# Kernel optimization log

Measured on AMD Instinct MI355X. Metric: run time of the kernel, lower is better.

## Reference

```python
import jax, jax.numpy as jnp
import numpy as np

N = 20000       # n_nodes
NHID = 256      # nhid_gcn
NOUT = 128      # gcn output / gru input
H = 128         # nout_gru
NHID_E = 256    # nhid_edges
T = 16          # snapshots (end_day - start_day + 1)
E = 320000      # edges per snapshot
EP = 100000     # edges to predict
BN_EPS = 1e-5


def setup_inputs() -> dict:
    key = jax.random.key(0)
    ks = jax.random.split(key, 20)
    s = 0.02
    return {
        "adj_rows": jax.random.randint(ks[0], (T, E), 0, N, dtype=jnp.int32),
        "adj_cols": jax.random.randint(ks[1], (T, E), 0, N, dtype=jnp.int32),
        "adj_vals": jax.random.uniform(ks[2], (T, E), dtype=jnp.float32),
        "edges": jax.random.randint(ks[3], (2, EP), 0, N, dtype=jnp.int32),
        # GCN params (layer0: nfeat=N -> NHID, layer1: NHID -> NOUT)
        "W0": jax.random.normal(ks[4], (N, NHID), jnp.float32) * s,
        "b0": jnp.zeros((NHID,), jnp.float32),
        "W1": jax.random.normal(ks[5], (NHID, NOUT), jnp.float32) * s,
        "b1": jnp.zeros((NOUT,), jnp.float32),
        # GRU params (torch layout: [3H, in], [3H, H])
        "W_ih": jax.random.normal(ks[6], (3 * H, NOUT), jnp.float32) * s,
        "W_hh": jax.random.normal(ks[7], (3 * H, H), jnp.float32) * s,
        "b_ih": jnp.zeros((3 * H,), jnp.float32),
        "b_hh": jnp.zeros((3 * H,), jnp.float32),
        # BatchNorm1d affine params
        "gamma": jnp.ones((H,), jnp.float32),
        "beta": jnp.zeros((H,), jnp.float32),
        # edge predictor MLP
        "We1": jax.random.normal(ks[8], (2 * H, NHID_E), jnp.float32) * s,
        "be1": jnp.full((NHID_E,), 0.01, jnp.float32),
        "We2": jax.random.normal(ks[9], (NHID_E, 2), jnp.float32) * s,
        "be2": jnp.full((2,), 0.01, jnp.float32),
    }


def reference(adj_rows, adj_cols, adj_vals, edges,
              W0, b0, W1, b1, W_ih, W_hh, b_ih, b_hh,
              gamma, beta, We1, be1, We2, be2):
    def spmm(rows, cols, vals, x):
        # (sparse adj) @ x via gather + segment_sum  -> [N, d]
        return jax.ops.segment_sum(vals[:, None] * x[cols], rows, num_segments=N)

    def gcn_step(rows, cols, vals):
        # layer 0: input is identity, so support = W0
        x = spmm(rows, cols, vals, W0) + b0
        x = jax.nn.relu(x)              # dropout p=0.0 -> no-op
        # layer 1 (output layer, no relu)
        x = spmm(rows, cols, vals, x @ W1) + b1
        return x

    out = jax.vmap(gcn_step)(adj_rows, adj_cols, adj_vals)  # [T, N, NOUT]

    # single-layer GRU over time, batch = nodes
    def gru_cell(h, x):
        gi = x @ W_ih.T + b_ih
        gh = h @ W_hh.T + b_hh
        i_r, i_z, i_n = jnp.split(gi, 3, axis=-1)
        h_r, h_z, h_n = jnp.split(gh, 3, axis=-1)
        r = jax.nn.sigmoid(i_r + h_r)
        z = jax.nn.sigmoid(i_z + h_z)
        n = jnp.tanh(i_n + r * h_n)
        return (1.0 - z) * n + z * h, None

    h0 = jnp.zeros((N, H), out.dtype)
    final_emb, _ = jax.lax.scan(gru_cell, h0, out)  # [N, H]

    # BatchNorm1d in training mode: batch (node) statistics, biased variance
    mean = final_emb.mean(axis=0)
    var = final_emb.var(axis=0)
    final_emb = (final_emb - mean) * jax.lax.rsqrt(var + BN_EPS) * gamma + beta

    nodes_first = final_emb[edges[0]]
    nodes_second = final_emb[edges[1]]
    hcat = jnp.concatenate([nodes_first, nodes_second], axis=1)  # [EP, 2H]
    hmid = jax.nn.relu(hcat @ We1 + be1)
    logits = hmid @ We2 + be2
    return jax.nn.log_softmax(logits, axis=1)
```

## Files before the change

### kernel.cpp

```cpp
#include <hip/hip_runtime.h>
#include <math.h>

#define N_NODES 20000
#define NHID    256
#define NOUT    128
#define HDIM    128
#define NHID_E  256
#define T_SNAP  16
#define E_EDGES 320000
#define EP_EDGES 100000
#define BN_EPS  1e-5f

#define BROWS 128
#define NBUCK 157
#define BCAP  4096
#define P1CHUNK 2048

typedef unsigned short u16;
typedef __attribute__((ext_vector_type(8))) short bf16x8;
typedef __attribute__((ext_vector_type(8))) unsigned short u16x8;
typedef __attribute__((ext_vector_type(4))) float f32x4;

__device__ __forceinline__ u16 f2b(float f) {
    unsigned u = __float_as_uint(f);
    u += 0x7FFFu + ((u >> 16) & 1u);
    return (u16)(u >> 16);
}
__device__ __forceinline__ float b2f(u16 s) { return __uint_as_float(((unsigned)s) << 16); }

__device__ __forceinline__ float fexp2(float x) {
#if __has_builtin(__builtin_amdgcn_exp2f)
    return __builtin_amdgcn_exp2f(x);
#else
    return exp2f(x);
#endif
}
__device__ __forceinline__ float frcp(float x) {
#if __has_builtin(__builtin_amdgcn_rcpf)
    return __builtin_amdgcn_rcpf(x);
#else
    return 1.f / x;
#endif
}
__device__ __forceinline__ float fsig(float x) {
    return frcp(1.f + fexp2(x * -1.4426950408889634f));
}
__device__ __forceinline__ float ftanh(float x) {
    float t = fexp2(x * 2.8853900817779268f);
    return 1.f - 2.f * frcp(t + 1.f);
}

#if __has_builtin(__builtin_amdgcn_fdot2_f32_bf16)
#define HAVE_DOT2 1
typedef __attribute__((ext_vector_type(2))) __bf16 bf2v;
__device__ __forceinline__ float dot2b(unsigned x, unsigned v, float acc) {
    return __builtin_amdgcn_fdot2_f32_bf16(
        __builtin_bit_cast(bf2v, x), __builtin_bit_cast(bf2v, v), acc, false);
}
__device__ __forceinline__ unsigned pack_lo(unsigned a, unsigned b) {
#if __has_builtin(__builtin_amdgcn_perm)
    return __builtin_amdgcn_perm(a, b, 0x01000504u);
#else
    return (a & 0xFFFFu) | (b << 16);
#endif
}
__device__ __forceinline__ unsigned pack_hi(unsigned a, unsigned b) {
#if __has_builtin(__builtin_amdgcn_perm)
    return __builtin_amdgcn_perm(a, b, 0x03020706u);
#else
    return (a >> 16) | (b & 0xFFFF0000u);
#endif
}
#else
#define HAVE_DOT2 0
#endif

__global__ __launch_bounds__(256) void k_p1(const int* __restrict__ rows,
        const int* __restrict__ cols, const float* __restrict__ vals,
        int* __restrict__ bcnt, uint2* __restrict__ staging,
        uint4* __restrict__ ovf, int* __restrict__ ovf_cnt) {
    int t = blockIdx.y;
    int base = blockIdx.x * P1CHUNK;
    int tid = threadIdx.x;
    __shared__ int hist[256], sc[256], excl[256], cursor[256], gbase[256];
    __shared__ uint2 ebuf[P1CHUNK];
    __shared__ u16 ebuck[P1CHUNK];
    hist[tid] = 0;
    __syncthreads();
    const int*   rt = rows + (size_t)t * E_EDGES;
    const int*   ct = cols + (size_t)t * E_EDGES;
    const float* vt = vals + (size_t)t * E_EDGES;
    #pragma unroll
    for (int k = 0; k < P1CHUNK / 256; ++k) {
        int i = base + k * 256 + tid;
        if (i < E_EDGES) atomicAdd(&hist[rt[i] >> 7], 1);
    }
    __syncthreads();
    sc[tid] = hist[tid];
    __syncthreads();
    for (int off = 1; off < 256; off <<= 1) {
        int add = (tid >= off) ? sc[tid - off] : 0;
        __syncthreads();
        sc[tid] += add;
        __syncthreads();
    }
    excl[tid]   = sc[tid] - hist[tid];
    cursor[tid] = sc[tid] - hist[tid];
    __syncthreads();
    #pragma unroll
    for (int k = 0; k < P1CHUNK / 256; ++k) {
        int i = base + k * 256 + tid;
        if (i < E_EDGES) {
            int r = rt[i];
            int b = r >> 7;
            int s = atomicAdd(&cursor[b], 1);
            uint2 e;
            e.x = (unsigned)ct[i] | ((unsigned)(r & 127) << 15);
            e.y = __float_as_uint(vt[i]);
            ebuf[s]  = e;
            ebuck[s] = (u16)b;
        }
    }
    __syncthreads();
    if (hist[tid] > 0) gbase[tid] = atomicAdd(&bcnt[t * NBUCK + tid], hist[tid]);
    __syncthreads();
    int nvalid = min(P1CHUNK, E_EDGES - base);
    for (int s = tid; s < nvalid; s += 256) {
        int b = ebuck[s];
        int g = gbase[b] + (s - excl[b]);
        if (g < BCAP) {
            staging[((size_t)t * NBUCK + b) * BCAP + g] = ebuf[s];
        } else {
            int o = atomicAdd(ovf_cnt, 1);
            uint4 e4; e4.x = (unsigned)(t * NBUCK + b); e4.y = ebuf[s].x; e4.z = ebuf[s].y; e4.w = 0;
            ovf[o] = e4;
        }
    }
}

__global__ void k_bscan(const int* __restrict__ bcnt, int* __restrict__ bbase,
                        int* __restrict__ row_ptr) {
    __shared__ int sh[256];
    __shared__ int carry;
    int tid = threadIdx.x;
    if (tid == 0) carry = 0;
    __syncthreads();
    for (int b0 = 0; b0 < T_SNAP * NBUCK; b0 += 256) {
        int i = b0 + tid;
        int v = (i < T_SNAP * NBUCK) ? bcnt[i] : 0;
        sh[tid] = v;
        __syncthreads();
        for (int off = 1; off < 256; off <<= 1) {
            int add = (tid >= off) ? sh[tid - off] : 0;
            __syncthreads();
            sh[tid] += add;
            __syncthreads();
        }
        if (i < T_SNAP * NBUCK) bbase[i] = carry + sh[tid] - v;
        __syncthreads();
        if (tid == 255) carry += sh[255];
        __syncthreads();
    }
    if (tid < T_SNAP) row_ptr[tid * (N_NODES + 1) + N_NODES] = E_EDGES;
}

__global__ __launch_bounds__(256) void k_p2(const int* __restrict__ bcnt,
        const int* __restrict__ bbase, const uint2* __restrict__ staging,
        const uint4* __restrict__ ovf, const int* __restrict__ ovf_cnt,
        uint2* __restrict__ colval, int* __restrict__ row_ptr) {
    int b = blockIdx.x, t = blockIdx.y, tid = threadIdx.x;
    int idx = t * NBUCK + b;
    int cnt = bcnt[idx];
    int gb  = bbase[idx];
    __shared__ int hist[BROWS], cursor[BROWS], sc[BROWS];
    if (tid < BROWS) hist[tid] = 0;
    __syncthreads();
    int staged = min(cnt, BCAP);
    const uint2* st = staging + (size_t)idx * BCAP;
    for (int s = tid; s < staged; s += 256)
        atomicAdd(&hist[st[s].x >> 15], 1);
    int nov = (cnt > staged) ? *ovf_cnt : 0;
    for (int o = tid; o < nov; o += 256) {
        uint4 e = ovf[o];
        if ((int)e.x == idx) atomicAdd(&hist[(e.y >> 15) & 127], 1);
    }
    __syncthreads();
    if (tid < BROWS) sc[tid] = hist[tid];
    __syncthreads();
    for (int off = 1; off < BROWS; off <<= 1) {
        int add = (tid < BROWS && tid >= off) ? sc[tid - off] : 0;
        __syncthreads();
        if (tid < BROWS) sc[tid] += add;
        __syncthreads();
    }
    if (tid < BROWS) {
        int ex = sc[tid] - hist[tid];
        cursor[tid] = ex;
        int row = b * BROWS + tid;
        if (row < N_NODES)
            row_ptr[t * (N_NODES + 1) + row] = gb - t * E_EDGES + ex;
    }
    __syncthreads();
    for (int s = tid; s < staged; s += 256) {
        uint2 e = st[s];
        int rl = e.x >> 15;
        int pos = atomicAdd(&cursor[rl], 1);
        uint2 o2; o2.x = e.x & 0x7FFF; o2.y = e.y;
        colval[(size_t)gb + pos] = o2;
    }
    for (int o = tid; o < nov; o += 256) {
        uint4 e = ovf[o];
        if ((int)e.x == idx) {
            int rl = (e.y >> 15) & 127;
            int pos = atomicAdd(&cursor[rl], 1);
            uint2 o2; o2.x = e.y & 0x7FFF; o2.y = e.z;
            colval[(size_t)gb + pos] = o2;
        }
    }
}

__global__ void k_cvt(const float* __restrict__ in, u16* __restrict__ out, int n4) {
    int i = blockIdx.x * 256 + threadIdx.x;
    if (i < n4) {
        float4 v = ((const float4*)in)[i];
        ushort4 o;
        o.x = f2b(v.x); o.y = f2b(v.y); o.z = f2b(v.z); o.w = f2b(v.w);
        ((ushort4*)out)[i] = o;
    }
}

__global__ void k_tcvt(const float* __restrict__ in, u16* __restrict__ out, int Kr, int Nc) {
    int i = blockIdx.x * 256 + threadIdx.x;
    if (i < Kr * Nc) {
        int k = i / Nc, n = i - k * Nc;
        out[(size_t)n * Kr + k] = f2b(in[i]);
    }
}

__global__ void k_build_bg(const float* __restrict__ Wih, const float* __restrict__ Whh,
                           u16* __restrict__ Bg) {
    int i = blockIdx.x * 256 + threadIdx.x;
    if (i >= 512 * 256) return;
    int rr = i >> 8, k = i & 255;
    int c = rr >> 4, u = rr & 15, g = c & 3, jj = ((c >> 2) << 4) + u;
    float v;
    if (g == 0)      v = (k < 128) ? Wih[(size_t)jj * 128 + k]         : Whh[(size_t)jj * 128 + k - 128];
    else if (g == 1) v = (k < 128) ? Wih[(size_t)(128 + jj) * 128 + k] : Whh[(size_t)(128 + jj) * 128 + k - 128];
    else if (g == 2) v = (k < 128) ? Wih[(size_t)(256 + jj) * 128 + k] : 0.f;
    else             v = (k < 128) ? 0.f : Whh[(size_t)(256 + jj) * 128 + k - 128];
    Bg[i] = f2b(v);
}

__global__ void k_build_bgb(const float* __restrict__ bih, const float* __restrict__ bhh,
                            float* __restrict__ bgb) {
    int rr = blockIdx.x * 256 + threadIdx.x;
    if (rr >= 512) return;
    int c = rr >> 4, u = rr & 15, g = c & 3, jj = ((c >> 2) << 4) + u;
    float v;
    if (g == 0)      v = bih[jj] + bhh[jj];
    else if (g == 1) v = bih[128 + jj] + bhh[128 + jj];
    else if (g == 2) v = bih[256 + jj];
    else             v = bhh[256 + jj];
    bgb[rr] = v;
}

template<bool RELU>
__global__ __launch_bounds__(256) void k_spmm0(
        const int* __restrict__ rp_all, const uint2* __restrict__ cv_all,
        int t0, const u16* __restrict__ X,
        const float* __restrict__ bias, u16* __restrict__ Out) {
    int lane = threadIdx.x & 63;
    int row = blockIdx.x * 4 + (threadIdx.x >> 6);
    int tl = blockIdx.y, t = t0 + tl;
    const int*   rp = rp_all + (size_t)t * (N_NODES + 1);
    const uint2* cv = cv_all + (size_t)t * E_EDGES;
    int hw = lane >> 5, l = lane & 31;
    int s = rp[row], e = rp[row + 1];
    int k = s + hw;
    uint2 a0 = make_uint2(0u, 0u), a1 = make_uint2(0u, 0u);
    if (k < e)     a0 = cv[k];
    if (k + 2 < e) a1 = cv[k + 2];
#if HAVE_DOT2
    float acc[8] = {};
    for (; k < e; k += 4) {
        uint2 c0 = a0, c1 = a1;
        bool ok1 = (k + 2) < e;
        int e1 = e - 1;
        a0 = cv[min(k + 4, e1)];
        a1 = cv[min(k + 6, e1)];
        unsigned col1 = ok1 ? c1.x : c0.x;
        float va1f = ok1 ? __uint_as_float(c1.y) : 0.f;
        unsigned vv = (unsigned)f2b(__uint_as_float(c0.y)) | ((unsigned)f2b(va1f) << 16);
        uint4 x0 = *(const uint4*)(X + (size_t)c0.x * NHID + l * 8);
        uint4 x1 = *(const uint4*)(X + (size_t)col1 * NHID + l * 8);
        acc[0] = dot2b(pack_lo(x0.x, x1.x), vv, acc[0]);
        acc[1] = dot2b(pack_hi(x0.x, x1.x), vv, acc[1]);
        acc[2] = dot2b(pack_lo(x0.y, x1.y), vv, acc[2]);
        acc[3] = dot2b(pack_hi(x0.y, x1.y), vv, acc[3]);
        acc[4] = dot2b(pack_lo(x0.z, x1.z), vv, acc[4]);
        acc[5] = dot2b(pack_hi(x0.z, x1.z), vv, acc[5]);
        acc[6] = dot2b(pack_lo(x0.w, x1.w), vv, acc[6]);
        acc[7] = dot2b(pack_hi(x0.w, x1.w), vv, acc[7]);
    }
    #pragma unroll
    for (int i = 0; i < 8; ++i) {
        float v = acc[i];
        v += __shfl_xor(v, 32);
        v += bias[l * 8 + i];
        acc[i] = RELU ? fmaxf(v, 0.f) : v;
    }
    float* accw = acc;
#else
    float acc0[8] = {}, acc1[8] = {};
    for (; k < e; k += 4) {
        uint2 c0 = a0, c1 = a1;
        bool ok1 = (k + 2) < e;
        int e1 = e - 1;
        a0 = cv[min(k + 4, e1)];
        a1 = cv[min(k + 6, e1)];
        float va0 = __uint_as_float(c0.y);
        float va1 = ok1 ? __uint_as_float(c1.y) : 0.f;
        unsigned col1 = ok1 ? c1.x : c0.x;
        u16x8 x0 = *(const u16x8*)(X + (size_t)c0.x * NHID + l * 8);
        u16x8 x1 = *(const u16x8*)(X + (size_t)col1 * NHID + l * 8);
        #pragma unroll
        for (int i = 0; i < 8; ++i) {
            acc0[i] = fmaf(va0, b2f(x0[i]), acc0[i]);
            acc1[i] = fmaf(va1, b2f(x1[i]), acc1[i]);
        }
    }
    #pragma unroll
    for (int i = 0; i < 8; ++i) {
        float v = acc0[i] + acc1[i];
        v += __shfl_xor(v, 32);
        v += bias[l * 8 + i];
        acc0[i] = RELU ? fmaxf(v, 0.f) : v;
    }
    float* accw = acc0;
#endif
    if (hw == 0) {
        u16x8 o;
        #pragma unroll
        for (int i = 0; i < 8; ++i) o[i] = f2b(accw[i]);
        *(u16x8*)(Out + ((size_t)tl * N_NODES + row) * NHID + l * 8) = o;
    }
}

template<bool RELU>
__global__ __launch_bounds__(256) void k_spmm1(
        const int* __restrict__ rp_all, const uint2* __restrict__ cv_all,
        int t0, const u16* __restrict__ X, size_t xtstride,
        const float* __restrict__ bias, u16* __restrict__ Out) {
    int lane = threadIdx.x & 63;
    int row = blockIdx.x * 4 + (threadIdx.x >> 6);
    int tl = blockIdx.y, t = t0 + tl;
    const int*   rp = rp_all + (size_t)t * (N_NODES + 1);
    const uint2* cv = cv_all + (size_t)t * E_EDGES;
    const u16*   Xt = X + xtstride * tl;
    int qw = lane >> 4, l = lane & 15;
    int s = rp[row], e = rp[row + 1];
    int k = s + qw;
    uint2 a0 = make_uint2(0u, 0u), a1 = make_uint2(0u, 0u);
    if (k < e)     a0 = cv[k];
    if (k + 4 < e) a1 = cv[k + 4];
#if HAVE_DOT2
    float acc[8] = {};
    for (; k < e; k += 8) {
        uint2 c0 = a0, c1 = a1;
        bool ok1 = (k + 4) < e;
        int e1 = e - 1;
        a0 = cv[min(k + 8, e1)];
        a1 = cv[min(k + 12, e1)];
        unsigned col1 = ok1 ? c1.x : c0.x;
        float va1f = ok1 ? __uint_as_float(c1.y) : 0.f;
        unsigned vv = (unsigned)f2b(__uint_as_float(c0.y)) | ((unsigned)f2b(va1f) << 16);
        uint4 x0 = *(const uint4*)(Xt + (size_t)c0.x * NOUT + l * 8);
        uint4 x1 = *(const uint4*)(Xt + (size_t)col1 * NOUT + l * 8);
        acc[0] = dot2b(pack_lo(x0.x, x1.x), vv, acc[0]);
        acc[1] = dot2b(pack_hi(x0.x, x1.x), vv, acc[1]);
        acc[2] = dot2b(pack_lo(x0.y, x1.y), vv, acc[2]);
        acc[3] = dot2b(pack_hi(x0.y, x1.y), vv, acc[3]);
        acc[4] = dot2b(pack_lo(x0.z, x1.z), vv, acc[4]);
        acc[5] = dot2b(pack_hi(x0.z, x1.z), vv, acc[5]);
        acc[6] = dot2b(pack_lo(x0.w, x1.w), vv, acc[6]);
        acc[7] = dot2b(pack_hi(x0.w, x1.w), vv, acc[7]);
    }
    #pragma unroll
    for (int i = 0; i < 8; ++i) {
        float v = acc[i];
        v += __shfl_xor(v, 32);
        v += __shfl_xor(v, 16);
        v += bias[l * 8 + i];
        acc[i] = RELU ? fmaxf(v, 0.f) : v;
    }
    float* accw = acc;
#else
    float acc0[8] = {}, acc1[8] = {};
    for (; k < e; k += 8) {
        uint2 c0 = a0, c1 = a1;
        bool ok1 = (k + 4) < e;
        int e1 = e - 1;
        a0 = cv[min(k + 8, e1)];
        a1 = cv[min(k + 12, e1)];
        float va0 = __uint_as_float(c0.y);
        float va1 = ok1 ? __uint_as_float(c1.y) : 0.f;
        unsigned col1 = ok1 ? c1.x : c0.x;
        u16x8 x0 = *(const u16x8*)(Xt + (size_t)c0.x * NOUT + l * 8);
        u16x8 x1 = *(const u16x8*)(Xt + (size_t)col1 * NOUT + l * 8);
        #pragma unroll
        for (int i = 0; i < 8; ++i) {
            acc0[i] = fmaf(va0, b2f(x0[i]), acc0[i]);
            acc1[i] = fmaf(va1, b2f(x1[i]), acc1[i]);
        }
    }
    #pragma unroll
    for (int i = 0; i < 8; ++i) {
        float v = acc0[i] + acc1[i];
        v += __shfl_xor(v, 32);
        v += __shfl_xor(v, 16);
        v += bias[l * 8 + i];
        acc0[i] = RELU ? fmaxf(v, 0.f) : v;
    }
    float* accw = acc0;
#endif
    if (qw == 0) {
        u16x8 o;
        #pragma unroll
        for (int i = 0; i < 8; ++i) o[i] = f2b(accw[i]);
        *(u16x8*)(Out + ((size_t)tl * N_NODES + row) * NOUT + l * 8) = o;
    }
}

template<int KC, bool BIAS>
__global__ __launch_bounds__(256) void k_mgemm(
        const u16* __restrict__ A, const u16* __restrict__ B, int ldb,
        const float* __restrict__ bias, u16* __restrict__ C, int ldc, int M) {
    constexpr int K = KC * 32;
    __shared__ bf16x8 frag[8 * KC * 64];
    int tid = threadIdx.x, lane = tid & 63, wave = tid >> 6;
    int m0 = blockIdx.y * 64, n0 = blockIdx.x * 128;

    for (int f = wave; f < 8 * KC; f += 4) {
        int nl = f / KC, kc = f % KC;
        frag[f * 64 + lane] = *(const bf16x8*)(B + (size_t)(n0 + nl * 16 + (lane & 15)) * ldb
                                               + kc * 32 + ((lane >> 4) << 3));
    }
    __syncthreads();

    int arow = m0 + wave * 16 + (lane & 15);
    bool rowok = arow < M;
    const u16* ap = A + (size_t)arow * K + ((lane >> 4) << 3);
    bf16x8 zf = {0, 0, 0, 0, 0, 0, 0, 0};
    bf16x8 af[KC];
    #pragma unroll
    for (int kc = 0; kc < KC; ++kc)
        af[kc] = rowok ? *(const bf16x8*)(ap + kc * 32) : zf;

    f32x4 acc[8] = {};
    #pragma unroll
    for (int kc = 0; kc < KC; ++kc)
        #pragma unroll
        for (int nl = 0; nl < 8; ++nl)
            acc[nl] = __builtin_amdgcn_mfma_f32_16x16x32_bf16(
                af[kc], frag[(nl * KC + kc) * 64 + lane], acc[nl], 0, 0, 0);

    int r0 = m0 + wave * 16 + ((lane >> 4) << 2);
    #pragma unroll
    for (int nl = 0; nl < 8; ++nl) {
        int col = n0 + nl * 16 + (lane & 15);
        float bv = BIAS ? bias[col] : 0.f;
        #pragma unroll
        for (int r = 0; r < 4; ++r) {
            int row = r0 + r;
            if (row < M) C[(size_t)row * ldc + col] = f2b(acc[nl][r] + bv);
        }
    }
}

__global__ __launch_bounds__(512, 2) void k_gru_fused2(
        const u16* __restrict__ X2_all, const u16* __restrict__ Bg,
        const float* __restrict__ bgb, float* __restrict__ H) {
    __shared__ u16 hbuf[2][32][132];
    int tid = threadIdx.x, lane = tid & 63, wave = tid >> 6;
    int q = wave >> 1, hb = wave & 1;
    int u = lane & 15, kgrp = lane >> 4;
    int m0 = blockIdx.x * 32;
    int jj = (2 * q + hb) * 16 + u;

    bf16x8 bfrag[4][8];
    #pragma unroll
    for (int g = 0; g < 4; ++g)
        #pragma unroll
        for (int kc = 0; kc < 8; ++kc)
            bfrag[g][kc] = *(const bf16x8*)(Bg
                + (size_t)(q * 128 + (4 * hb + g) * 16 + u) * 256
                + kc * 32 + kgrp * 8);

    float bR = bgb[q * 128 + (4 * hb + 0) * 16 + u];
    float bZ = bgb[q * 128 + (4 * hb + 1) * 16 + u];
    float bI = bgb[q * 128 + (4 * hb + 2) * 16 + u];
    float bH = bgb[q * 128 + (4 * hb + 3) * 16 + u];

    for (int i = tid; i < 32 * 132; i += 512) ((u16*)hbuf[0])[i] = 0;

    float hstate[2][4] = {};
    __syncthreads();

    for (int t = 0; t < T_SNAP; ++t) {
        const u16* X2t = X2_all + (size_t)t * N_NODES * NOUT;
        int rb = t & 1, wb = rb ^ 1;
        #pragma unroll
        for (int tile = 0; tile < 2; ++tile) {
            int arow = m0 + tile * 16 + u;
            bf16x8 afx[4], afh[4];
            const u16* a1 = X2t + (size_t)arow * 128 + kgrp * 8;
            #pragma unroll
            for (int kc = 0; kc < 4; ++kc)
                afx[kc] = *(const bf16x8*)(a1 + kc * 32);
            #pragma unroll
            for (int kc = 0; kc < 4; ++kc)
                afh[kc] = *(const bf16x8*)&hbuf[rb][tile * 16 + u][kc * 32 + kgrp * 8];

            f32x4 acc[4] = {};
            #pragma unroll
            for (int kc = 0; kc < 4; ++kc)
                #pragma unroll
                for (int g = 0; g < 4; ++g)
                    acc[g] = __builtin_amdgcn_mfma_f32_16x16x32_bf16(
                        afx[kc], bfrag[g][kc], acc[g], 0, 0, 0);
            #pragma unroll
            for (int kc = 0; kc < 4; ++kc)
                #pragma unroll
                for (int g = 0; g < 4; ++g)
                    acc[g] = __builtin_amdgcn_mfma_f32_16x16x32_bf16(
                        afh[kc], bfrag[g][4 + kc], acc[g], 0, 0, 0);

            #pragma unroll
            for (int r = 0; r < 4; ++r) {
                int lrow = tile * 16 + kgrp * 4 + r;
                float rg = fsig(acc[0][r] + bR);
                float zg = fsig(acc[1][r] + bZ);
                float ng = ftanh(acc[2][r] + bI + rg * (acc[3][r] + bH));
                float hn = (1.f - zg) * ng + zg * hstate[tile][r];
                hstate[tile][r] = hn;
                hbuf[wb][lrow][jj] = f2b(hn);
            }
        }
        __syncthreads();
    }
    #pragma unroll
    for (int tile = 0; tile < 2; ++tile)
        #pragma unroll
        for (int r = 0; r < 4; ++r) {
            int row = m0 + tile * 16 + kgrp * 4 + r;
            H[(size_t)row * HDIM + jj] = hstate[tile][r];
        }
}

__global__ void k_bnstats(const float* __restrict__ h, float* __restrict__ stats) {
    int j = threadIdx.x;
    int r0 = blockIdx.x * 200;
    float s = 0.f, sq = 0.f;
    for (int r = r0; r < r0 + 200; ++r) {
        float v = h[(size_t)r * HDIM + j];
        s += v; sq += v * v;
    }
    atomicAdd(&stats[j], s);
    atomicAdd(&stats[128 + j], sq);
}

__global__ void k_bnapply(const float* __restrict__ h, const float* __restrict__ stats,
                          const float* __restrict__ gamma, const float* __restrict__ beta,
                          u16* __restrict__ emb) {
    int i = blockIdx.x * 256 + threadIdx.x;
    if (i >= N_NODES * HDIM) return;
    int j = i & 127;
    float mean = stats[j] * (1.f / N_NODES);
    float var  = stats[128 + j] * (1.f / N_NODES) - mean * mean;
    emb[i] = f2b((h[i] - mean) * rsqrtf(var + BN_EPS) * gamma[j] + beta[j]);
}

__global__ __launch_bounds__(256) void k_edge(const int* __restrict__ edges,
        const u16* __restrict__ P, const u16* __restrict__ Q,
        const float* __restrict__ We2, const float* __restrict__ be2,
        float* __restrict__ out) {
    int e = blockIdx.x * 4 + (threadIdx.x >> 6);
    int lane = threadIdx.x & 63;
    if (e >= EP_EDGES) return;
    int u = edges[e];
    int v = edges[EP_EDGES + e];
    ushort4 pv = *(const ushort4*)(P + (size_t)u * NHID_E + lane * 4);
    ushort4 qv = *(const ushort4*)(Q + (size_t)v * NHID_E + lane * 4);
    const float4* w = (const float4*)(We2 + lane * 8);
    float4 w0 = w[0], w1 = w[1];
    float h0 = fmaxf(b2f(pv.x) + b2f(qv.x), 0.f);
    float h1 = fmaxf(b2f(pv.y) + b2f(qv.y), 0.f);
    float h2 = fmaxf(b2f(pv.z) + b2f(qv.z), 0.f);
    float h3 = fmaxf(b2f(pv.w) + b2f(qv.w), 0.f);
    float l0 = h0 * w0.x + h1 * w0.z + h2 * w1.x + h3 * w1.z;
    float l1 = h0 * w0.y + h1 * w0.w + h2 * w1.y + h3 * w1.w;
    #pragma unroll
    for (int off = 32; off > 0; off >>= 1) {
        l0 += __shfl_down(l0, off);
        l1 += __shfl_down(l1, off);
    }
    if (lane == 0) {
        l0 += be2[0]; l1 += be2[1];
        float m = fmaxf(l0, l1);
        float lse = m + logf(expf(l0 - m) + expf(l1 - m));
        out[(size_t)e * 2 + 0] = l0 - lse;
        out[(size_t)e * 2 + 1] = l1 - lse;
    }
}

extern "C" void kernel_launch(void* const* d_in, const int* in_sizes, int n_in,
                              void* d_out, int out_size, void* d_ws, size_t ws_size,
                              hipStream_t stream) {
    const int*   adj_rows = (const int*)  d_in[0];
    const int*   adj_cols = (const int*)  d_in[1];
    const float* adj_vals = (const float*)d_in[2];
    const int*   edges    = (const int*)  d_in[3];
    const float* W0   = (const float*)d_in[4];
    const float* b0   = (const float*)d_in[5];
    const float* W1   = (const float*)d_in[6];
    const float* b1   = (const float*)d_in[7];
    const float* W_ih = (const float*)d_in[8];
    const float* W_hh = (const float*)d_in[9];
    const float* b_ih = (const float*)d_in[10];
    const float* b_hh = (const float*)d_in[11];
    const float* gamma = (const float*)d_in[12];
    const float* beta  = (const float*)d_in[13];
    const float* We1  = (const float*)d_in[14];
    const float* be1  = (const float*)d_in[15];
    const float* We2  = (const float*)d_in[16];
    const float* be2  = (const float*)d_in[17];
    float* out = (float*)d_out;

    char* ws = (char*)d_ws;
    size_t off = 0;
    auto alloc = [&](size_t bytes) -> void* {
        void* p = ws + off;
        off += (bytes + 255) & ~(size_t)255;
        return p;
    };
    int*   row_ptr = (int*)  alloc((size_t)T_SNAP * (N_NODES + 1) * 4);
    uint2* colval  = (uint2*)alloc((size_t)T_SNAP * E_EDGES * 8);
    u16*   W0_bf   = (u16*)  alloc((size_t)N_NODES * NHID * 2);
    u16*   W1t     = (u16*)  alloc((size_t)NOUT * NHID * 2);
    u16*   We1T    = (u16*)  alloc((size_t)NHID_E * 256 * 2);
    u16*   BgB     = (u16*)  alloc((size_t)512 * 256 * 2);
    float* bgbB    = (float*)alloc(512 * 4);
    float* h       = (float*)alloc((size_t)N_NODES * HDIM * 4);
    float* stats   = (float*)alloc(256 * 4);
    int*   bcnt    = (int*)  alloc((size_t)T_SNAP * NBUCK * 4);
    int*   bbase   = (int*)  alloc((size_t)T_SNAP * NBUCK * 4);
    int*   ovf_cnt = (int*)  alloc(256);
    size_t mark = off;

    off = mark;
    uint2* staging = (uint2*)alloc((size_t)T_SNAP * NBUCK * BCAP * 8);
    uint4* ovf     = (uint4*)alloc((size_t)T_SNAP * E_EDGES * 16);
    size_t csr_end = off;

    int BT = 8;
    u16 *X0_b, *Y_b, *X2_all;
    size_t comp_end;
    for (;;) {
        off = mark;
        X0_b   = (u16*)alloc((size_t)BT * N_NODES * NHID * 2);
        Y_b    = (u16*)alloc((size_t)BT * N_NODES * NOUT * 2);
        X2_all = (u16*)alloc((size_t)T_SNAP * N_NODES * NOUT * 2);
        comp_end = off;
        if (comp_end <= ws_size || BT == 4) break;
        BT >>= 1;
    }

    off = mark;
    u16* emb = (u16*)alloc((size_t)N_NODES * HDIM * 2);
    u16* P   = (u16*)alloc((size_t)N_NODES * NHID_E * 2);
    u16* Q   = (u16*)alloc((size_t)N_NODES * NHID_E * 2);
    size_t post_end = off;

    size_t need = csr_end;
    if (comp_end > need) need = comp_end;
    if (post_end > need) need = post_end;
    if (need > ws_size) return;

    hipMemsetAsync(bcnt,    0, (size_t)T_SNAP * NBUCK * 4, stream);
    hipMemsetAsync(ovf_cnt, 0, 256, stream);
    hipMemsetAsync(stats,   0, 256 * 4, stream);

    dim3 p1g((E_EDGES + P1CHUNK - 1) / P1CHUNK, T_SNAP);
    k_p1   <<<p1g, 256, 0, stream>>>(adj_rows, adj_cols, adj_vals, bcnt, staging, ovf, ovf_cnt);
    k_bscan<<<1, 256, 0, stream>>>(bcnt, bbase, row_ptr);
    k_p2   <<<dim3(NBUCK, T_SNAP), 256, 0, stream>>>(bcnt, bbase, staging, ovf, ovf_cnt,
                                                     colval, row_ptr);

    k_cvt      <<<(N_NODES * NHID / 4 + 255) / 256, 256, 0, stream>>>(W0, W0_bf, N_NODES * NHID / 4);
    k_tcvt     <<<(NHID * NOUT + 255) / 256,  256, 0, stream>>>(W1, W1t, NHID, NOUT);
    k_tcvt     <<<(256 * NHID_E + 255) / 256, 256, 0, stream>>>(We1, We1T, 256, NHID_E);
    k_build_bg <<<(512 * 256 + 255) / 256, 256, 0, stream>>>(W_ih, W_hh, BgB);
    k_build_bgb<<<2, 256, 0, stream>>>(b_ih, b_hh, bgbB);

    for (int g = 0; g < T_SNAP; g += BT) {
        k_spmm0<true><<<dim3(N_NODES / 4, BT), 256, 0, stream>>>(
            row_ptr, colval, g, W0_bf, b0, X0_b);
        int M = BT * N_NODES;
        k_mgemm<8, false><<<dim3(1, (M + 63) / 64), 256, 0, stream>>>(
            X0_b, W1t, NHID, nullptr, Y_b, NOUT, M);
        k_spmm1<false><<<dim3(N_NODES / 4, BT), 256, 0, stream>>>(
            row_ptr, colval, g, Y_b, (size_t)N_NODES * NOUT, b1,
            X2_all + (size_t)g * N_NODES * NOUT);
    }

    k_gru_fused2<<<N_NODES / 32, 512, 0, stream>>>(X2_all, BgB, bgbB, h);

    k_bnstats<<<100, 128, 0, stream>>>(h, stats);
    k_bnapply<<<(N_NODES * HDIM + 255) / 256, 256, 0, stream>>>(h, stats, gamma, beta, emb);

    k_mgemm<4, true><<<dim3(2, (N_NODES + 63) / 64), 256, 0, stream>>>(
        emb, We1T, 256, be1, P, NHID_E, N_NODES);
    k_mgemm<4, false><<<dim3(2, (N_NODES + 63) / 64), 256, 0, stream>>>(
        emb, We1T + 128, 256, nullptr, Q, NHID_E, N_NODES);
    k_edge<<<(EP_EDGES + 3) / 4, 256, 0, stream>>>(edges, P, Q, We2, be2, out);
}
```

Before: 877.3 us.

## Halve GRU block rows and prefetch next-timestep input fragments

The fused GRU kernel now processes 16 rows per block instead of 32, doubling the grid to 1250 blocks. The X input fragments for timestep t+1 are loaded into registers while the current step's MFMAs and gate math run, so global-load latency overlaps the serial recurrence. In exchange, each block reloads the full gate-weight fragment set for half as many rows, which doubles total weight-load traffic.

```diff
diff --git a/kernel.cpp b/kernel.cpp
--- a/kernel.cpp
+++ b/kernel.cpp
@@ -480,11 +480,11 @@
 __global__ __launch_bounds__(512, 2) void k_gru_fused2(
         const u16* __restrict__ X2_all, const u16* __restrict__ Bg,
         const float* __restrict__ bgb, float* __restrict__ H) {
-    __shared__ u16 hbuf[2][32][132];
+    __shared__ u16 hbuf[2][16][132];
     int tid = threadIdx.x, lane = tid & 63, wave = tid >> 6;
     int q = wave >> 1, hb = wave & 1;
     int u = lane & 15, kgrp = lane >> 4;
-    int m0 = blockIdx.x * 32;
+    int m0 = blockIdx.x * 16;
     int jj = (2 * q + hb) * 16 + u;
 
     bf16x8 bfrag[4][8];
@@ -501,60 +501,69 @@
     float bI = bgb[q * 128 + (4 * hb + 2) * 16 + u];
     float bH = bgb[q * 128 + (4 * hb + 3) * 16 + u];
 
-    for (int i = tid; i < 32 * 132; i += 512) ((u16*)hbuf[0])[i] = 0;
-
-    float hstate[2][4] = {};
+    for (int i = tid; i < 16 * 132; i += 512) ((u16*)hbuf[0])[i] = 0;
+
+    float hstate[4] = {};
+    int arow = m0 + u;
+    const u16* aptr = X2_all + (size_t)arow * 128 + kgrp * 8;
+
+    bf16x8 afx[4];
+    #pragma unroll
+    for (int kc = 0; kc < 4; ++kc)
+        afx[kc] = *(const bf16x8*)(aptr + kc * 32);
     __syncthreads();
 
     for (int t = 0; t < T_SNAP; ++t) {
-        const u16* X2t = X2_all + (size_t)t * N_NODES * NOUT;
         int rb = t & 1, wb = rb ^ 1;
-        #pragma unroll
-        for (int tile = 0; tile < 2; ++tile) {
-            int arow = m0 + tile * 16 + u;
-            bf16x8 afx[4], afh[4];
-            const u16* a1 = X2t + (size_t)arow * 128 + kgrp * 8;
+        bf16x8 afh[4];
+        #pragma unroll
+        for (int kc = 0; kc < 4; ++kc)
+            afh[kc] = *(const bf16x8*)&hbuf[rb][u][kc * 32 + kgrp * 8];
+
+        f32x4 acc[4] = {};
+        #pragma unroll
+        for (int kc = 0; kc < 4; ++kc)
+            #pragma unroll
+            for (int g = 0; g < 4; ++g)
+                acc[g] = __builtin_amdgcn_mfma_f32_16x16x32_bf16(
+                    afx[kc], bfrag[g][kc], acc[g], 0, 0, 0);
+        #pragma unroll
+        for (int kc = 0; kc < 4; ++kc)
+            #pragma unroll
+            for (int g = 0; g < 4; ++g)
+                acc[g] = __builtin_amdgcn_mfma_f32_16x16x32_bf16(
+                    afh[kc], bfrag[g][4 + kc], acc[g], 0, 0, 0);
+
+        bf16x8 afn[4];
+        if (t + 1 < T_SNAP) {
+            const u16* ap2 = aptr + (size_t)(t + 1) * N_NODES * 128;
             #pragma unroll
             for (int kc = 0; kc < 4; ++kc)
-                afx[kc] = *(const bf16x8*)(a1 + kc * 32);
+                afn[kc] = *(const bf16x8*)(ap2 + kc * 32);
+        } else {
             #pragma unroll
-            for (int kc = 0; kc < 4; ++kc)
-                afh[kc] = *(const bf16x8*)&hbuf[rb][tile * 16 + u][kc * 32 + kgrp * 8];
-
-            f32x4 acc[4] = {};
-            #pragma unroll
-            for (int kc = 0; kc < 4; ++kc)
-                #pragma unroll
-                for (int g = 0; g < 4; ++g)
-                    acc[g] = __builtin_amdgcn_mfma_f32_16x16x32_bf16(
-                        afx[kc], bfrag[g][kc], acc[g], 0, 0, 0);
-            #pragma unroll
-            for (int kc = 0; kc < 4; ++kc)
-                #pragma unroll
-                for (int g = 0; g < 4; ++g)
-                    acc[g] = __builtin_amdgcn_mfma_f32_16x16x32_bf16(
-                        afh[kc], bfrag[g][4 + kc], acc[g], 0, 0, 0);
-
-            #pragma unroll
-            for (int r = 0; r < 4; ++r) {
-                int lrow = tile * 16 + kgrp * 4 + r;
-                float rg = fsig(acc[0][r] + bR);
-                float zg = fsig(acc[1][r] + bZ);
-                float ng = ftanh(acc[2][r] + bI + rg * (acc[3][r] + bH));
-                float hn = (1.f - zg) * ng + zg * hstate[tile][r];
-                hstate[tile][r] = hn;
-                hbuf[wb][lrow][jj] = f2b(hn);
-            }
+            for (int kc = 0; kc < 4; ++kc) afn[kc] = afx[kc];
+        }
+
+        #pragma unroll
+        for (int r = 0; r < 4; ++r) {
+            int lrow = kgrp * 4 + r;
+            float rg = fsig(acc[0][r] + bR);
+            float zg = fsig(acc[1][r] + bZ);
+            float ng = ftanh(acc[2][r] + bI + rg * (acc[3][r] + bH));
+            float hn = (1.f - zg) * ng + zg * hstate[r];
+            hstate[r] = hn;
+            hbuf[wb][lrow][jj] = f2b(hn);
         }
         __syncthreads();
-    }
-    #pragma unroll
-    for (int tile = 0; tile < 2; ++tile)
-        #pragma unroll
-        for (int r = 0; r < 4; ++r) {
-            int row = m0 + tile * 16 + kgrp * 4 + r;
-            H[(size_t)row * HDIM + jj] = hstate[tile][r];
-        }
+        #pragma unroll
+        for (int kc = 0; kc < 4; ++kc) afx[kc] = afn[kc];
+    }
+    #pragma unroll
+    for (int r = 0; r < 4; ++r) {
+        int row = m0 + kgrp * 4 + r;
+        H[(size_t)row * HDIM + jj] = hstate[r];
+    }
 }
 
 __global__ void k_bnstats(const float* __restrict__ h, float* __restrict__ stats) {
@@ -713,7 +722,7 @@
             X2_all + (size_t)g * N_NODES * NOUT);
     }
 
-    k_gru_fused2<<<N_NODES / 32, 512, 0, stream>>>(X2_all, BgB, bgbB, h);
+    k_gru_fused2<<<N_NODES / 16, 512, 0, stream>>>(X2_all, BgB, bgbB, h);
 
     k_bnstats<<<100, 128, 0, stream>>>(h, stats);
     k_bnapply<<<(N_NODES * HDIM + 255) / 256, 256, 0, stream>>>(h, stats, gamma, beta, emb);
```

Result: faster. 816.7 us (-6.9%).
